# Kernel optimization log

Hardware: AMD Instinct MI355X
Metric: run time of the kernel (lower is better)

Reference implementation:

```python
import jax, jax.numpy as jnp
import numpy as np

N_ENT = 50000
N_REL = 500
IN_DIM = 128
OUT_DIM = 128
N_EDGES = 500000
LRELU_SLOPE = 0.01  # torch F.leaky_relu default


def setup_inputs() -> dict:
    key = jax.random.key(0)
    ks = jax.random.split(key, 8)
    # triplets [3, E]: row0=src entity, row1=relation, row2=dst entity.
    # Ensure every entity appears as a source so no 0/0 in the edge-softmax division.
    src_extra = jax.random.randint(ks[0], (N_EDGES - N_ENT,), 0, N_ENT)
    src = jnp.concatenate([jnp.arange(N_ENT), src_extra])
    rel = jax.random.randint(ks[1], (N_EDGES,), 0, N_REL)
    dst = jax.random.randint(ks[2], (N_EDGES,), 0, N_ENT)
    triplets = jnp.stack([src, rel, dst]).astype(jnp.int64)
    ent_embed = jax.random.normal(ks[3], (N_ENT, IN_DIM), dtype=jnp.float32)
    rel_embed = jax.random.normal(ks[4], (N_REL, IN_DIM), dtype=jnp.float32)
    adj = jax.random.randint(ks[5], (2, N_EDGES), 0, N_ENT).astype(jnp.int64)  # unused by forward
    # Xavier-normal (gain=1.414) init for the two linear layers, like the torch module.
    std_a = 1.414 * np.sqrt(2.0 / (3 * IN_DIM + OUT_DIM))
    std_a2 = 1.414 * np.sqrt(2.0 / (OUT_DIM + 1))
    W_a = jax.random.normal(ks[6], (3 * IN_DIM, OUT_DIM), dtype=jnp.float32) * std_a
    b_a = jnp.zeros((OUT_DIM,), dtype=jnp.float32)
    W_a2 = jax.random.normal(ks[7], (OUT_DIM, 1), dtype=jnp.float32) * std_a2
    b_a2 = jnp.zeros((1,), dtype=jnp.float32)
    return {"triplets": triplets, "ent_embed": ent_embed, "rel_embed": rel_embed,
            "adj": adj, "W_a": W_a, "b_a": b_a, "W_a2": W_a2, "b_a2": b_a2}


def reference(triplets, ent_embed, rel_embed, adj, W_a, b_a, W_a2, b_a2):
    src, rel, dst = triplets[0], triplets[1], triplets[2]
    n_ent = ent_embed.shape[0]
    # Gather + concat: [E, 3*in_dim]
    h = jnp.concatenate([ent_embed[src], rel_embed[rel], ent_embed[dst]], axis=1)
    c = h @ W_a + b_a                                   # [E, out_dim]
    b = jax.nn.leaky_relu(c @ W_a2 + b_a2, LRELU_SLOPE)  # [E, 1]
    e_b = jnp.exp(b)                                    # [E, 1]
    # Sparse edge-softmax grouped by source node (sparse.sum over dst dim).
    denom = jax.ops.segment_sum(e_b, src, num_segments=n_ent)        # [N, 1]
    numer = jax.ops.segment_sum(e_b * c, src, num_segments=n_ent)    # [N, out_dim]
    out = numer / denom
    return jax.nn.elu(out)  # concat=True branch
```

## Files before the change

kernel.cpp:

```cpp
#include <hip/hip_runtime.h>

#define DIM 128

typedef __attribute__((ext_vector_type(8))) short bf16x8;
typedef __attribute__((ext_vector_type(4))) float f32x4;

__device__ inline unsigned short to_bf16(float f) {
    unsigned u = __float_as_uint(f);
    u = (u + 0x7FFFu + ((u >> 16) & 1u)) >> 16;
    return (unsigned short)u;
}
__device__ inline unsigned pack_bf16(float lo, float hi) {
    return (unsigned)to_bf16(lo) | ((unsigned)to_bf16(hi) << 16);
}
__device__ inline float unpack_lo(unsigned v) { return __uint_as_float(v << 16); }
__device__ inline float unpack_hi(unsigned v) { return __uint_as_float(v & 0xFFFF0000u); }

__global__ void wprep_kernel(const float* __restrict__ W_a, unsigned short* __restrict__ Wt,
                             int* __restrict__ counts, int n) {
    const int c = blockIdx.x;
    const int k = threadIdx.x;
    const int srow = (c < 128) ? k : (256 + k);
    const int scol = (c < 128) ? c : (c - 128);
    Wt[c * DIM + k] = to_bf16(W_a[srow * DIM + scol]);
    for (int i = blockIdx.x * 128 + k; i < n; i += 256 * 128) counts[i] = 0;
}

__global__ __launch_bounds__(256) void stage1_kernel(
        const float* __restrict__ ent, const float* __restrict__ rel,
        const int* __restrict__ T, const unsigned short* __restrict__ Wt,
        const float* __restrict__ W_rel, const float* __restrict__ b_a,
        const float* __restrict__ Wa2,
        unsigned* __restrict__ P1h, unsigned* __restrict__ P3h, unsigned* __restrict__ P2h,
        float* __restrict__ q1, float* __restrict__ q3, float* __restrict__ q2,
        int* __restrict__ counts, int NE, int NR, int E, int NT2, int HB, int RB) {
    __shared__ unsigned smem[4288];
    int b = blockIdx.x;
    const int t = threadIdx.x;

    if (b < HB) {
        for (int e = b * 256 + t; e < E; e += HB * 256)
            atomicAdd(&counts[T[e]], 1);
        return;
    }
    b -= HB;

    if (b < RB) {
        float* xs   = (float*)smem;
        float* sred = (float*)(smem + 1024);
        const int row0 = b * 8;
        #pragma unroll
        for (int e = 0; e < 8; ++e) {
            int row = row0 + e;
            xs[e * DIM + t % DIM + (t / DIM) * 0] = 0.0f;
        }
        const int half = t >> 7;
        const int tc   = t & 127;
        #pragma unroll
        for (int e = 0; e < 4; ++e) {
            int row = row0 + half * 4 + e;
            xs[(half * 4 + e) * DIM + tc] = (row < NR) ? rel[(size_t)row * DIM + tc] : 0.0f;
        }
        __syncthreads();
        float acc[4] = {0.f, 0.f, 0.f, 0.f};
        #pragma unroll 4
        for (int k = 0; k < DIM; ++k) {
            const float wv = W_rel[k * DIM + tc];
            #pragma unroll
            for (int e = 0; e < 4; ++e) acc[e] += xs[(half * 4 + e) * DIM + k] * wv;
        }
        const float wa2 = Wa2[tc];
        const int lane = t & 63;
        #pragma unroll
        for (int e = 0; e < 4; ++e) {
            float v = acc[e] * wa2;
            #pragma unroll
            for (int o = 32; o > 0; o >>= 1) v += __shfl_down(v, o);
            if (lane == 0) sred[(half * 4 + e) * 2 + ((t >> 6) & 1)] = v;
        }
        __syncthreads();
        #pragma unroll
        for (int e = 0; e < 4; ++e) {
            int row = row0 + half * 4 + e;
            float hi = __shfl_down(acc[e], 1);
            if (row < NR && (tc & 1) == 0)
                P2h[(size_t)row * 64 + (tc >> 1)] = pack_bf16(acc[e], hi);
        }
        if (t < 8) {
            int row = row0 + t;
            if (row < NR) q2[row] = sred[t * 2] + sred[t * 2 + 1];
        }
        return;
    }
    b -= RB;

    const int wave = t >> 6;
    const int tile2 = b * 4 + wave;
    const bool active = tile2 < NT2;
    const int lane = t & 63;
    const int g = lane >> 4;
    const int m = lane & 15;
    unsigned short* lds16 = (unsigned short*)smem + wave * 2080;
    unsigned* lds32 = smem + wave * 1040;
    int half = 0, row0 = 0;
    unsigned* Ph = P1h;
    if (active) {
        half = tile2 & 1;
        row0 = (tile2 >> 1) * 16;
        Ph = half ? P3h : P1h;
        float* qo = half ? q3 : q1;
        const unsigned short* Wh = Wt + half * 128 * DIM;

        const int rowA = min(row0 + m, NE - 1);
        const float* arow = ent + (size_t)rowA * DIM;
        bf16x8 afrag[4];
        #pragma unroll
        for (int kk = 0; kk < 4; ++kk) {
            const float4 u0 = *(const float4*)(arow + kk * 32 + g * 8);
            const float4 u1 = *(const float4*)(arow + kk * 32 + g * 8 + 4);
            bf16x8 a;
            a[0] = (short)to_bf16(u0.x); a[1] = (short)to_bf16(u0.y);
            a[2] = (short)to_bf16(u0.z); a[3] = (short)to_bf16(u0.w);
            a[4] = (short)to_bf16(u1.x); a[5] = (short)to_bf16(u1.y);
            a[6] = (short)to_bf16(u1.z); a[7] = (short)to_bf16(u1.w);
            afrag[kk] = a;
        }

        float qp[4] = {0.f, 0.f, 0.f, 0.f};
        #pragma unroll
        for (int ct = 0; ct < 8; ++ct) {
            f32x4 acc = {0.f, 0.f, 0.f, 0.f};
            #pragma unroll
            for (int kk = 0; kk < 4; ++kk) {
                const bf16x8 bb = *(const bf16x8*)(Wh + (ct * 16 + m) * DIM + kk * 32 + g * 8);
                acc = __builtin_amdgcn_mfma_f32_16x16x32_bf16(afrag[kk], bb, acc, 0, 0, 0);
            }
            const int c = ct * 16 + m;
            const float bias = half ? 0.0f : b_a[c];
            const float wa2  = Wa2[c];
            #pragma unroll
            for (int r = 0; r < 4; ++r) {
                const float v = acc[r] + bias;
                qp[r] += v * wa2;
                lds16[(g * 4 + r) * 130 + c] = to_bf16(v);
            }
        }

        #pragma unroll
        for (int r = 0; r < 4; ++r) {
            float v = qp[r];
            #pragma unroll
            for (int o = 1; o < 16; o <<= 1) v += __shfl_xor(v, o);
            const int row = row0 + g * 4 + r;
            if (m == 0 && row < NE) qo[row] = v;
        }
    }
    __syncthreads();
    if (active) {
        #pragma unroll
        for (int i = 0; i < 16; ++i) {
            const int row = row0 + i;
            if (row < NE) Ph[(size_t)row * 64 + lane] = lds32[i * 65 + lane];
        }
    }
}

__device__ inline int wave_incl_scan(int v) {
    const int lane = threadIdx.x & 63;
    #pragma unroll
    for (int o = 1; o < 64; o <<= 1) {
        int u = __shfl_up(v, o);
        if (lane >= o) v += u;
    }
    return v;
}

__global__ void scan_bsum_kernel(const int* __restrict__ counts, int* __restrict__ bsum, int n) {
    const int t = threadIdx.x;
    const int base = blockIdx.x * 1024 + t * 4;
    int s = 0;
    #pragma unroll
    for (int j = 0; j < 4; ++j) if (base + j < n) s += counts[base + j];
    #pragma unroll
    for (int o = 32; o > 0; o >>= 1) s += __shfl_down(s, o);
    __shared__ int ws[4];
    if ((t & 63) == 0) ws[t >> 6] = s;
    __syncthreads();
    if (t == 0) bsum[blockIdx.x] = ws[0] + ws[1] + ws[2] + ws[3];
}

__global__ void scan_write_kernel(const int* __restrict__ counts, const int* __restrict__ bsum,
                                  int* __restrict__ offsets, int* __restrict__ cursor,
                                  int n, int total, int nb) {
    __shared__ int s_boff;
    __shared__ int wsum[4], wpre[4];
    const int t = threadIdx.x;
    if (t < 64) {
        int v = (t < nb) ? bsum[t] : 0;
        int incl = wave_incl_scan(v);
        int ex = incl - v;
        int want = __shfl(ex, (int)blockIdx.x);
        if (t == 0) s_boff = want;
    }
    const int base = blockIdx.x * 1024 + t * 4;
    int c[4];
    int s = 0;
    #pragma unroll
    for (int j = 0; j < 4; ++j) {
        c[j] = (base + j < n) ? counts[base + j] : 0;
        s += c[j];
    }
    int incl = wave_incl_scan(s);
    const int wid = t >> 6, lane = t & 63;
    if (lane == 63) wsum[wid] = incl;
    __syncthreads();
    if (t == 0) {
        int run = 0;
        #pragma unroll
        for (int k = 0; k < 4; ++k) { wpre[k] = run; run += wsum[k]; }
    }
    __syncthreads();
    int run = incl - s + wpre[wid] + s_boff;
    #pragma unroll
    for (int j = 0; j < 4; ++j) {
        if (base + j < n) { offsets[base + j] = run; cursor[base + j] = run; run += c[j]; }
    }
    if (base == 0 && blockIdx.x == 0) offsets[n] = total;
}

__global__ void scatter_kernel(const int* __restrict__ T, const float* __restrict__ q1,
                               const float* __restrict__ q2, const float* __restrict__ q3,
                               const float* __restrict__ b_a2, int* __restrict__ cursor,
                               uint2* __restrict__ rdw, int E) {
    const int e = blockIdx.x * blockDim.x + threadIdx.x;
    if (e >= E) return;
    const int s = T[e], r = T[E + e], d = T[2 * E + e];
    float b = q1[s] + q2[r] + q3[d] + b_a2[0];
    b = (b > 0.0f) ? b : 0.01f * b;
    const float wv = __expf(b);
    const int pos = atomicAdd(&cursor[s], 1);
    rdw[pos] = make_uint2(((unsigned)r << 17) | (unsigned)d, __float_as_uint(wv));
}

__global__ void gather_kernel(const int* __restrict__ offsets, const uint2* __restrict__ rdw,
                              const unsigned* __restrict__ P1h, const unsigned* __restrict__ P2h,
                              const unsigned* __restrict__ P3h, float* __restrict__ out, int n) {
    const int node = (blockIdx.x << 2) + (threadIdx.x >> 6);
    if (node >= n) return;
    const int lane = threadIdx.x & 63;
    const int lo = offsets[node], hi = offsets[node + 1];
    float axp[4] = {0.f,0.f,0.f,0.f};
    float ayp[4] = {0.f,0.f,0.f,0.f};
    float wsp[4] = {0.f,0.f,0.f,0.f};
    int i = lo;
    for (; i + 3 < hi; i += 4) {
        uint2 e[4];
        #pragma unroll
        for (int j = 0; j < 4; ++j) e[j] = rdw[i + j];
        unsigned v2[4], v3[4];
        #pragma unroll
        for (int j = 0; j < 4; ++j) {
            v2[j] = P2h[(size_t)(e[j].x >> 17) * 64 + lane];
            v3[j] = P3h[(size_t)(e[j].x & 0x1FFFFu) * 64 + lane];
        }
        #pragma unroll
        for (int j = 0; j < 4; ++j) {
            const float wv = __uint_as_float(e[j].y);
            axp[j] += wv * (unpack_lo(v2[j]) + unpack_lo(v3[j]));
            ayp[j] += wv * (unpack_hi(v2[j]) + unpack_hi(v3[j]));
            wsp[j] += wv;
        }
    }
    for (; i < hi; ++i) {
        const uint2 e0 = rdw[i];
        const unsigned v2a = P2h[(size_t)(e0.x >> 17) * 64 + lane];
        const unsigned v3a = P3h[(size_t)(e0.x & 0x1FFFFu) * 64 + lane];
        const float wv = __uint_as_float(e0.y);
        axp[0] += wv * (unpack_lo(v2a) + unpack_lo(v3a));
        ayp[0] += wv * (unpack_hi(v2a) + unpack_hi(v3a));
        wsp[0] += wv;
    }
    const float ax = (axp[0] + axp[1]) + (axp[2] + axp[3]);
    const float ay = (ayp[0] + ayp[1]) + (ayp[2] + ayp[3]);
    const float inv = 1.0f / ((wsp[0] + wsp[1]) + (wsp[2] + wsp[3]));
    const unsigned p1 = P1h[(size_t)node * 64 + lane];
    float v0 = unpack_lo(p1) + ax * inv;
    float v1 = unpack_hi(p1) + ay * inv;
    v0 = (v0 > 0.0f) ? v0 : (__expf(v0) - 1.0f);
    v1 = (v1 > 0.0f) ? v1 : (__expf(v1) - 1.0f);
    *(float2*)(out + (size_t)node * DIM + (lane << 1)) = make_float2(v0, v1);
}

extern "C" void kernel_launch(void* const* d_in, const int* in_sizes, int n_in,
                              void* d_out, int out_size, void* d_ws, size_t ws_size,
                              hipStream_t stream) {
    const int*   T    = (const int*)d_in[0];
    const float* ent  = (const float*)d_in[1];
    const float* rel  = (const float*)d_in[2];
    const float* W_a  = (const float*)d_in[4];
    const float* b_a  = (const float*)d_in[5];
    const float* W_a2 = (const float*)d_in[6];
    const float* b_a2 = (const float*)d_in[7];
    float* out = (float*)d_out;

    const int E  = in_sizes[0] / 3;
    const int NE = in_sizes[1] / DIM;
    const int NR = in_sizes[2] / DIM;
    const int NB = (NE + 1023) / 1024;
    const int NT2 = ((NE + 15) / 16) * 2;
    const int HB = 256;
    const int RB = (NR + 7) / 8;
    const int PB = (NT2 + 3) / 4;

    float* ws = (float*)d_ws;
    size_t off = 0;
    unsigned* P1h = (unsigned*)(ws + off); off += (size_t)NE * 64;
    unsigned* P3h = (unsigned*)(ws + off); off += (size_t)NE * 64;
    unsigned* P2h = (unsigned*)(ws + off); off += (size_t)NR * 64;
    unsigned short* Wt = (unsigned short*)(ws + off); off += 256 * DIM / 2;
    float* q1   = ws + off; off += NE;
    float* q3   = ws + off; off += NE;
    float* q2   = ws + off; off += NR + 64;
    int* counts  = (int*)(ws + off); off += NE;
    int* offsets = (int*)(ws + off); off += NE + 64;
    int* cursor  = (int*)(ws + off); off += NE;
    int* bsum    = (int*)(ws + off); off += 64;
    uint2* rdw   = (uint2*)(ws + off); off += (size_t)E * 2;

    wprep_kernel<<<256, 128, 0, stream>>>(W_a, Wt, counts, NE);

    stage1_kernel<<<HB + RB + PB, 256, 0, stream>>>(
        ent, rel, T, Wt, W_a + 128 * DIM, b_a, W_a2,
        P1h, P3h, P2h, q1, q3, q2, counts, NE, NR, E, NT2, HB, RB);

    scan_bsum_kernel<<<NB, 256, 0, stream>>>(counts, bsum, NE);
    scan_write_kernel<<<NB, 256, 0, stream>>>(counts, bsum, offsets, cursor, NE, E, NB);

    scatter_kernel<<<(E + 255) / 256, 256, 0, stream>>>(T, q1, q2, q3, b_a2, cursor, rdw, E);

    gather_kernel<<<(NE + 3) / 4, 256, 0, stream>>>(offsets, rdw, P1h, P2h, P3h, out, NE);
}
```

Baseline: 122.6 us.

## Retile entity GEMM to 128-row blocks with LDS-staged swizzled A tiles

The entity projection GEMM moves from one 16-row tile per wave to 128-row blocks. Each block converts its entity rows to bf16 into swizzled shared memory, and each wave computes a 32x128 output tile, so every W fragment load now feeds two MFMAs. GEMM blocks are scheduled first, before the histogram and relation blocks, and launch bounds ask for 4 blocks per SM. The price is a larger LDS footprint (about 33KB), more accumulator registers, and coarser blocks that leave a tail across 782 blocks.

```diff
diff --git a/kernel.cpp b/kernel.cpp
--- a/kernel.cpp
+++ b/kernel.cpp
@@ -26,17 +26,98 @@
     for (int i = blockIdx.x * 128 + k; i < n; i += 256 * 128) counts[i] = 0;
 }
 
-__global__ __launch_bounds__(256) void stage1_kernel(
+__global__ __launch_bounds__(256, 4) void stage1_kernel(
         const float* __restrict__ ent, const float* __restrict__ rel,
         const int* __restrict__ T, const unsigned short* __restrict__ Wt,
         const float* __restrict__ W_rel, const float* __restrict__ b_a,
         const float* __restrict__ Wa2,
         unsigned* __restrict__ P1h, unsigned* __restrict__ P3h, unsigned* __restrict__ P2h,
         float* __restrict__ q1, float* __restrict__ q3, float* __restrict__ q2,
-        int* __restrict__ counts, int NE, int NR, int E, int NT2, int HB, int RB) {
-    __shared__ unsigned smem[4288];
+        int* __restrict__ counts, int NE, int NR, int E, int GB, int HB, int RB) {
+    __shared__ unsigned smem[8320];
     int b = blockIdx.x;
     const int t = threadIdx.x;
+
+    if (b < GB) {
+        const int half = b & 1;
+        const int mrow = (b >> 1) * 128;
+
+        #pragma unroll 4
+        for (int i = 0; i < 16; ++i) {
+            const int idx = i * 256 + t;
+            const int row = idx >> 5;
+            const int f4  = idx & 31;
+            const int rg  = min(mrow + row, NE - 1);
+            const float4 u = *(const float4*)(ent + (size_t)rg * DIM + f4 * 4);
+            const unsigned d0 = pack_bf16(u.x, u.y);
+            const unsigned d1 = pack_bf16(u.z, u.w);
+            const int dw = (f4 * 2) ^ ((row & 7) << 2);
+            *(uint2*)&smem[row * 64 + dw] = make_uint2(d0, d1);
+        }
+        __syncthreads();
+
+        const int wv = t >> 6, lane = t & 63;
+        const int g = lane >> 4, m = lane & 15;
+        const unsigned short* Wh = Wt + half * 128 * DIM;
+
+        f32x4 acc[2][8];
+        #pragma unroll
+        for (int rt = 0; rt < 2; ++rt)
+            #pragma unroll
+            for (int ct = 0; ct < 8; ++ct) acc[rt][ct] = (f32x4){0.f, 0.f, 0.f, 0.f};
+
+        #pragma unroll
+        for (int kk = 0; kk < 4; ++kk) {
+            const int dwa = (kk * 16 + g * 4) ^ ((m & 7) << 2);
+            const bf16x8 a0 = *(const bf16x8*)&smem[(wv * 32 + m) * 64 + dwa];
+            const bf16x8 a1 = *(const bf16x8*)&smem[(wv * 32 + 16 + m) * 64 + dwa];
+            #pragma unroll
+            for (int ct = 0; ct < 8; ++ct) {
+                const bf16x8 bb = *(const bf16x8*)(Wh + (ct * 16 + m) * DIM + kk * 32 + g * 8);
+                acc[0][ct] = __builtin_amdgcn_mfma_f32_16x16x32_bf16(a0, bb, acc[0][ct], 0, 0, 0);
+                acc[1][ct] = __builtin_amdgcn_mfma_f32_16x16x32_bf16(a1, bb, acc[1][ct], 0, 0, 0);
+            }
+        }
+        __syncthreads();
+
+        unsigned* __restrict__ Ph = half ? P3h : P1h;
+        float*    __restrict__ qo = half ? q3  : q1;
+        unsigned short* lds16 = (unsigned short*)smem;
+
+        #pragma unroll
+        for (int rt = 0; rt < 2; ++rt) {
+            float qp[4] = {0.f, 0.f, 0.f, 0.f};
+            #pragma unroll
+            for (int ct = 0; ct < 8; ++ct) {
+                const int c = ct * 16 + m;
+                const float bias = half ? 0.0f : b_a[c];
+                const float wa2  = Wa2[c];
+                #pragma unroll
+                for (int r = 0; r < 4; ++r) {
+                    const float v = acc[rt][ct][r] + bias;
+                    qp[r] += v * wa2;
+                    lds16[(wv * 32 + rt * 16 + g * 4 + r) * 130 + c] = to_bf16(v);
+                }
+            }
+            #pragma unroll
+            for (int r = 0; r < 4; ++r) {
+                float v = qp[r];
+                #pragma unroll
+                for (int o = 1; o < 16; o <<= 1) v += __shfl_xor(v, o);
+                const int row = mrow + wv * 32 + rt * 16 + g * 4 + r;
+                if (m == 0 && row < NE) qo[row] = v;
+            }
+        }
+        __syncthreads();
+        for (int i = 0; i < 32; ++i) {
+            const int linear = i * 256 + t;
+            const int row = linear >> 6, d = linear & 63;
+            const int rg = mrow + row;
+            if (rg < NE) Ph[(size_t)rg * 64 + d] = smem[row * 65 + d];
+        }
+        return;
+    }
+    b -= GB;
 
     if (b < HB) {
         for (int e = b * 256 + t; e < E; e += HB * 256)
@@ -45,15 +126,10 @@
     }
     b -= HB;
 
-    if (b < RB) {
+    {
         float* xs   = (float*)smem;
         float* sred = (float*)(smem + 1024);
         const int row0 = b * 8;
-        #pragma unroll
-        for (int e = 0; e < 8; ++e) {
-            int row = row0 + e;
-            xs[e * DIM + t % DIM + (t / DIM) * 0] = 0.0f;
-        }
         const int half = t >> 7;
         const int tc   = t & 127;
         #pragma unroll
@@ -89,78 +165,6 @@
         if (t < 8) {
             int row = row0 + t;
             if (row < NR) q2[row] = sred[t * 2] + sred[t * 2 + 1];
-        }
-        return;
-    }
-    b -= RB;
-
-    const int wave = t >> 6;
-    const int tile2 = b * 4 + wave;
-    const bool active = tile2 < NT2;
-    const int lane = t & 63;
-    const int g = lane >> 4;
-    const int m = lane & 15;
-    unsigned short* lds16 = (unsigned short*)smem + wave * 2080;
-    unsigned* lds32 = smem + wave * 1040;
-    int half = 0, row0 = 0;
-    unsigned* Ph = P1h;
-    if (active) {
-        half = tile2 & 1;
-        row0 = (tile2 >> 1) * 16;
-        Ph = half ? P3h : P1h;
-        float* qo = half ? q3 : q1;
-        const unsigned short* Wh = Wt + half * 128 * DIM;
-
-        const int rowA = min(row0 + m, NE - 1);
-        const float* arow = ent + (size_t)rowA * DIM;
-        bf16x8 afrag[4];
-        #pragma unroll
-        for (int kk = 0; kk < 4; ++kk) {
-            const float4 u0 = *(const float4*)(arow + kk * 32 + g * 8);
-            const float4 u1 = *(const float4*)(arow + kk * 32 + g * 8 + 4);
-            bf16x8 a;
-            a[0] = (short)to_bf16(u0.x); a[1] = (short)to_bf16(u0.y);
-            a[2] = (short)to_bf16(u0.z); a[3] = (short)to_bf16(u0.w);
-            a[4] = (short)to_bf16(u1.x); a[5] = (short)to_bf16(u1.y);
-            a[6] = (short)to_bf16(u1.z); a[7] = (short)to_bf16(u1.w);
-            afrag[kk] = a;
-        }
-
-        float qp[4] = {0.f, 0.f, 0.f, 0.f};
-        #pragma unroll
-        for (int ct = 0; ct < 8; ++ct) {
-            f32x4 acc = {0.f, 0.f, 0.f, 0.f};
-            #pragma unroll
-            for (int kk = 0; kk < 4; ++kk) {
-                const bf16x8 bb = *(const bf16x8*)(Wh + (ct * 16 + m) * DIM + kk * 32 + g * 8);
-                acc = __builtin_amdgcn_mfma_f32_16x16x32_bf16(afrag[kk], bb, acc, 0, 0, 0);
-            }
-            const int c = ct * 16 + m;
-            const float bias = half ? 0.0f : b_a[c];
-            const float wa2  = Wa2[c];
-            #pragma unroll
-            for (int r = 0; r < 4; ++r) {
-                const float v = acc[r] + bias;
-                qp[r] += v * wa2;
-                lds16[(g * 4 + r) * 130 + c] = to_bf16(v);
-            }
-        }
-
-        #pragma unroll
-        for (int r = 0; r < 4; ++r) {
-            float v = qp[r];
-            #pragma unroll
-            for (int o = 1; o < 16; o <<= 1) v += __shfl_xor(v, o);
-            const int row = row0 + g * 4 + r;
-            if (m == 0 && row < NE) qo[row] = v;
-        }
-    }
-    __syncthreads();
-    if (active) {
-        #pragma unroll
-        for (int i = 0; i < 16; ++i) {
-            const int row = row0 + i;
-            if (row < NE) Ph[(size_t)row * 64 + lane] = lds32[i * 65 + lane];
         }
     }
 }
@@ -307,10 +311,9 @@
     const int NE = in_sizes[1] / DIM;
     const int NR = in_sizes[2] / DIM;
     const int NB = (NE + 1023) / 1024;
-    const int NT2 = ((NE + 15) / 16) * 2;
+    const int GB = ((NE + 127) / 128) * 2;
     const int HB = 256;
     const int RB = (NR + 7) / 8;
-    const int PB = (NT2 + 3) / 4;
 
     float* ws = (float*)d_ws;
     size_t off = 0;
@@ -329,9 +332,9 @@
 
     wprep_kernel<<<256, 128, 0, stream>>>(W_a, Wt, counts, NE);
 
-    stage1_kernel<<<HB + RB + PB, 256, 0, stream>>>(
+    stage1_kernel<<<GB + HB + RB, 256, 0, stream>>>(
         ent, rel, T, Wt, W_a + 128 * DIM, b_a, W_a2,
-        P1h, P3h, P2h, q1, q3, q2, counts, NE, NR, E, NT2, HB, RB);
+        P1h, P3h, P2h, q1, q3, q2, counts, NE, NR, E, GB, HB, RB);
 
     scan_bsum_kernel<<<NB, 256, 0, stream>>>(counts, bsum, NE);
     scan_write_kernel<<<NB, 256, 0, stream>>>(counts, bsum, offsets, cursor, NE, E, NB);
```

Measured after the change: 111.8 us. 1.1x faster.
